# Performance work log

Hardware: AMD Instinct MI355X
Metric: run time of the kernel (lower is better)

The kernel has to match this reference:

```python
import jax, jax.numpy as jnp
import numpy as np

B, N, M, D, NH, HD = 2, 1024, 1024, 1536, 16, 96
RD = HD // 3  # per-axis rotary dim = 32
EPS = 1e-6
SCALE = HD ** -0.5


def _rmsnorm(y, w):
    return y * jax.lax.rsqrt(jnp.mean(y * y, axis=-1, keepdims=True) + EPS) * w


def _rope_tables(T, H, W):
    # inv_freqs identical for t/h/w since all three dims are RD
    inv_f = 1.0 / (10000.0 ** (jnp.arange(0, RD, 2, dtype=jnp.float32)[: RD // 2] / RD))
    gt, gh, gw = jnp.meshgrid(
        jnp.arange(T, dtype=jnp.float32),
        jnp.arange(H, dtype=jnp.float32),
        jnp.arange(W, dtype=jnp.float32),
        indexing='ij')
    ft = gt.reshape(-1, 1) * inv_f[None, :]  # [L, RD//2]
    fh = gh.reshape(-1, 1) * inv_f[None, :]
    fw = gw.reshape(-1, 1) * inv_f[None, :]
    return (jnp.cos(ft), jnp.sin(ft), jnp.cos(fh), jnp.sin(fh), jnp.cos(fw), jnp.sin(fw))


def _apply_rope(xq, cos, sin):
    # xq: [B, L, NH, RD]; cos/sin: [L, RD//2]
    c = jnp.concatenate([cos, cos], axis=-1)[None, :, None, :]
    s = jnp.concatenate([sin, sin], axis=-1)[None, :, None, :]
    x1, x2 = jnp.split(xq, 2, axis=-1)
    rot = jnp.concatenate([-x2, x1], axis=-1)
    return xq * c + rot * s


def setup_inputs() -> dict:
    key = jax.random.key(0)
    ks = jax.random.split(key, 10)
    w = lambda k: jax.random.normal(k, (D, D), dtype=jnp.float32) * 0.02
    return {
        'cond': jax.random.normal(ks[0], (B, N, D), dtype=jnp.float32),
        'x': jax.random.normal(ks[1], (B, M, D), dtype=jnp.float32),
        'cond_q_w': w(ks[2]), 'cond_k_w': w(ks[3]), 'cond_v_w': w(ks[4]),
        'cond_qnorm_w': jnp.ones((D,), jnp.float32),
        'cond_knorm_w': jnp.ones((D,), jnp.float32),
        'cond_proj_w': w(ks[5]),
        'x_q_w': w(ks[6]), 'x_k_w': w(ks[7]), 'x_v_w': w(ks[8]),
        'x_qnorm_w': jnp.ones((D,), jnp.float32),
        'x_knorm_w': jnp.ones((D,), jnp.float32),
        'x_proj_w': w(ks[9]),
        'T': 2, 'H': 32, 'W': 32,
    }


def reference(cond, x, cond_q_w, cond_k_w, cond_v_w, cond_qnorm_w, cond_knorm_w,
              cond_proj_w, x_q_w, x_k_w, x_v_w, x_qnorm_w, x_knorm_w, x_proj_w,
              T, H, W):
    # dual-stream QKV + RMSNorm (qkv_bias=False, eval -> no dropout)
    cq = _rmsnorm(cond @ cond_q_w, cond_qnorm_w).reshape(B, N, NH, HD)
    ck = _rmsnorm(cond @ cond_k_w, cond_knorm_w).reshape(B, N, NH, HD)
    cv = (cond @ cond_v_w).reshape(B, N, NH, HD)
    xq = _rmsnorm(x @ x_q_w, x_qnorm_w).reshape(B, M, NH, HD)
    xk = _rmsnorm(x @ x_k_w, x_knorm_w).reshape(B, M, NH, HD)
    xv = (x @ x_v_w).reshape(B, M, NH, HD)

    q = jnp.concatenate([cq, xq], axis=1)  # [B, N+M, NH, HD]
    k = jnp.concatenate([ck, xk], axis=1)
    v = jnp.concatenate([cv, xv], axis=1)

    # 3D RoPE: split head_dim into t/h/w thirds and rotate each with its own freqs
    cos_t, sin_t, cos_h, sin_h, cos_w, sin_w = _rope_tables(T, H, W)
    qt, qh, qw = jnp.split(q, 3, axis=-1)
    kt, kh, kw = jnp.split(k, 3, axis=-1)
    q = jnp.concatenate([_apply_rope(qt, cos_t, sin_t),
                         _apply_rope(qh, cos_h, sin_h),
                         _apply_rope(qw, cos_w, sin_w)], axis=-1)
    k = jnp.concatenate([_apply_rope(kt, cos_t, sin_t),
                         _apply_rope(kh, cos_h, sin_h),
                         _apply_rope(kw, cos_w, sin_w)], axis=-1)

    # joint non-causal SDPA
    scores = jnp.einsum('blhd,bmhd->bhlm', q, k) * SCALE
    attn = jax.nn.softmax(scores, axis=-1)
    out = jnp.einsum('bhlm,bmhd->blhd', attn, v).reshape(B, N + M, D)

    cond_out = out[:, :N] @ cond_proj_w
    x_out = out[:, N:] @ x_proj_w
    return cond_out, x_out
```

## Files before the change

kernel.cpp:

```cpp
#include <hip/hip_runtime.h>
#include <stdint.h>

#define DEV __device__ __forceinline__

using f32x4  = __attribute__((ext_vector_type(4))) float;
using f32x16 = __attribute__((ext_vector_type(16))) float;
using bf16x8 = __attribute__((ext_vector_type(8))) short;

DEV ushort f2bf(float f){
  uint32_t u = __float_as_uint(f);
  u += 0x7FFFu + ((u >> 16) & 1u);
  return (ushort)(u >> 16);
}
DEV float bf2f(ushort h){ return __uint_as_float(((uint32_t)h) << 16); }

DEV void async16(const void* g, void* l){
  __builtin_amdgcn_global_load_lds(
      (const __attribute__((address_space(1))) void*)g,
      (__attribute__((address_space(3))) void*)l, 16, 0, 0);
}

union FU { uint4 u; bf16x8 v; };
DEV bf16x8 as_bf16x8(uint a, uint b, uint c, uint d){ FU f; f.u = make_uint4(a,b,c,d); return f.v; }

__global__ __launch_bounds__(256) void k_conv_in(const float* __restrict__ src, ushort* __restrict__ dst){
  int i = (blockIdx.x * 256 + threadIdx.x) * 8;
  float4 a = *(const float4*)(src + i);
  float4 b = *(const float4*)(src + i + 4);
  union { ushort s[8]; uint4 q; } o;
  o.s[0]=f2bf(a.x); o.s[1]=f2bf(a.y); o.s[2]=f2bf(a.z); o.s[3]=f2bf(a.w);
  o.s[4]=f2bf(b.x); o.s[5]=f2bf(b.y); o.s[6]=f2bf(b.z); o.s[7]=f2bf(b.w);
  *(uint4*)(dst + i) = o.q;
}

__global__ __launch_bounds__(256) void k_transpose_w(
    const float* w0, const float* w1, const float* w2, const float* w3,
    const float* w4, const float* w5, const float* w6, const float* w7,
    ushort* __restrict__ dst){
  __shared__ float tile[32][33];
  int z = blockIdx.z;
  const float* src = (z==0)?w0:(z==1)?w1:(z==2)?w2:(z==3)?w3:(z==4)?w4:(z==5)?w5:(z==6)?w6:w7;
  int n0 = blockIdx.x * 32;
  int k0 = blockIdx.y * 32;
  int tx = threadIdx.x;
  int ty = threadIdx.y;
  for (int j = 0; j < 4; ++j)
    tile[ty + j*8][tx] = src[(size_t)(k0 + ty + j*8) * 1536 + n0 + tx];
  __syncthreads();
  ushort* d = dst + (size_t)z * 1536 * 1536;
  for (int j = 0; j < 4; ++j){
    int n = n0 + ty + j*8;
    int k = k0 + tx;
    d[(size_t)n * 1536 + k] = f2bf(tile[tx][ty + j*8]);
  }
}

__global__ __launch_bounds__(512, 2) void k_gemm_qkv(const ushort* __restrict__ inb,
                                                     const ushort* __restrict__ Wt,
                                                     ushort* __restrict__ Y){
  __shared__ ushort As[2][16384];
  __shared__ ushort Bs[2][18432];
  int f = blockIdx.x;
  int nid = (f & 7) * 32 + (f >> 3);
  int z = nid >> 7; int r = nid & 127;
  int my = (r >> 2) & 7, nx = (r >> 5) * 4 + (r & 3);
  const ushort* A = inb + (size_t)z * 2048 * 1536 + (size_t)(my * 256) * 1536;
  const ushort* B = Wt  + (size_t)z * 4608 * 1536 + (size_t)(nx * 288) * 1536;
  ushort* Yt = Y + (size_t)z * 2048 * 4608 + (size_t)(my * 256) * 4608 + nx * 288;
  int tid = threadIdx.x;
  int w = tid >> 6, lane = tid & 63;
  int g = lane >> 4, fr = lane & 15;
  int wm = (w >> 1) * 64, wn = (w & 1) * 144;

  f32x4 acc[4][9] = {};

  auto stageA = [&](int b, int kt){
#pragma unroll
    for (int s = 0; s < 4; ++s){
      int c = s * 512 + tid;
      int row = c >> 3, ch = c & 7;
      async16(A + (size_t)row * 1536 + kt + ((ch ^ (row & 7)) * 8), &As[b][(s*512 + w*64) * 8]);
    }
  };
  auto stageB = [&](int b, int kt){
#pragma unroll
    for (int s = 0; s < 4; ++s){
      int c = s * 512 + tid;
      int row = c >> 3, ch = c & 7;
      async16(B + (size_t)row * 1536 + kt + ((ch ^ (row & 7)) * 8), &Bs[b][(s*512 + w*64) * 8]);
    }
    if (tid < 256){
      int c = 2048 + tid;
      int row = c >> 3, ch = c & 7;
      async16(B + (size_t)row * 1536 + kt + ((ch ^ (row & 7)) * 8), &Bs[b][(2048 + w*64) * 8]);
    }
  };

  stageA(0, 0); stageB(0, 0);
  asm volatile("s_waitcnt vmcnt(0)" ::: "memory");
  __builtin_amdgcn_s_barrier();
  asm volatile("" ::: "memory");

  for (int t = 0; t < 24; ++t){
    int cur = t & 1; int kt1 = (t + 1) * 64;
#pragma unroll
    for (int ks = 0; ks < 2; ++ks){
      bf16x8 af[4], bf[9];
#pragma unroll
      for (int j = 0; j < 4; ++j){
        int row = wm + j*16 + fr;
        af[j] = *(const bf16x8*)&As[cur][(row*8 + ((ks*4 + g) ^ (row & 7))) * 8];
      }
#pragma unroll
      for (int ni = 0; ni < 9; ++ni){
        int row = wn + ni*16 + fr;
        bf[ni] = *(const bf16x8*)&Bs[cur][(row*8 + ((ks*4 + g) ^ (row & 7))) * 8];
      }
      if (t < 23){
        if (ks == 0) stageA(cur ^ 1, kt1);
        else stageB(cur ^ 1, kt1);
      }
      asm volatile("" ::: "memory");
      __builtin_amdgcn_s_barrier();
      asm volatile("" ::: "memory");
      __builtin_amdgcn_s_setprio(1);
#pragma unroll
      for (int ni = 0; ni < 9; ++ni){
#pragma unroll
        for (int j = 0; j < 4; ++j)
          acc[j][ni] = __builtin_amdgcn_mfma_f32_16x16x32_bf16(af[j], bf[ni], acc[j][ni], 0, 0, 0);
      }
      __builtin_amdgcn_s_setprio(0);
      if (ks == 1) asm volatile("s_waitcnt vmcnt(0)" ::: "memory");
      asm volatile("" ::: "memory");
      __builtin_amdgcn_s_barrier();
      asm volatile("" ::: "memory");
    }
  }

#pragma unroll
  for (int mi = 0; mi < 4; ++mi)
#pragma unroll
    for (int ni = 0; ni < 9; ++ni)
#pragma unroll
      for (int rr = 0; rr < 4; ++rr)
        Yt[(size_t)(wm + mi*16 + g*4 + rr) * 4608 + wn + ni*16 + fr] = f2bf(acc[mi][ni][rr]);
}

template<bool OUT_BF16>
DEV void gemm_tile(const ushort* __restrict__ A, const ushort* __restrict__ Bt, void* __restrict__ Cp,
                   int K, int lda, int ldb, int ldc, int m0, int n0){
  __shared__ ushort As[8192];
  __shared__ ushort Bs[8192];
  int tid = threadIdx.x;
  int w = tid >> 6, lane = tid & 63;
  int g = lane >> 4, fr = lane & 15;
  int wm = (w >> 1) * 64, wn = (w & 1) * 64;
  f32x4 acc[4][4] = {};
  for (int kt = 0; kt < K; kt += 64){
    __syncthreads();
#pragma unroll
    for (int i = 0; i < 4; ++i){
      int ci = i * 256 + tid;
      int row = ci >> 3, ch = ci & 7;
      int src8 = (ch ^ (row & 7)) * 8;
      async16(A  + (size_t)(m0 + row) * lda + kt + src8, As + (i*256 + w*64) * 8);
      async16(Bt + (size_t)(n0 + row) * ldb + kt + src8, Bs + (i*256 + w*64) * 8);
    }
    __syncthreads();
#pragma unroll
    for (int ks = 0; ks < 2; ++ks){
      bf16x8 af[4], bf[4];
      int cidx = ((ks*4 + g) ^ (fr & 7)) * 8;
#pragma unroll
      for (int mi = 0; mi < 4; ++mi) af[mi] = *(const bf16x8*)(As + (wm + mi*16 + fr) * 64 + cidx);
#pragma unroll
      for (int ni = 0; ni < 4; ++ni) bf[ni] = *(const bf16x8*)(Bs + (wn + ni*16 + fr) * 64 + cidx);
#pragma unroll
      for (int mi = 0; mi < 4; ++mi)
#pragma unroll
        for (int ni = 0; ni < 4; ++ni)
          acc[mi][ni] = __builtin_amdgcn_mfma_f32_16x16x32_bf16(af[mi], bf[ni], acc[mi][ni], 0, 0, 0);
    }
  }
  int cr = (lane >> 4) * 4, cc2 = lane & 15;
#pragma unroll
  for (int mi = 0; mi < 4; ++mi)
#pragma unroll
    for (int ni = 0; ni < 4; ++ni)
#pragma unroll
      for (int r = 0; r < 4; ++r){
        size_t idx = (size_t)(m0 + wm + mi*16 + cr + r) * ldc + (n0 + wn + ni*16 + cc2);
        if (OUT_BF16) ((ushort*)Cp)[idx] = f2bf(acc[mi][ni][r]);
        else          ((float*)Cp)[idx]  = acc[mi][ni][r];
      }
}

__global__ __launch_bounds__(256) void k_gemm_proj(const ushort* __restrict__ AO, const ushort* __restrict__ Wtp,
                                                   float* __restrict__ out){
  int f = blockIdx.x;
  int nid = (f & 7) * 48 + (f >> 3);
  int z = nid / 96; int rr = nid - z * 96;
  int by = rr / 12; int bx = rr - by * 12;
  int s = z >> 1, bb = z & 1;
  gemm_tile<false>(AO + (size_t)(bb*2048 + s*1024) * 1536, Wtp + (size_t)s * 1536 * 1536,
                   (void*)(out + (size_t)(s*2048 + bb*1024) * 1536), 1536, 1536, 1536, 1536,
                   by * 128, bx * 128);
}

__global__ __launch_bounds__(256) void k_norm_rope(
    const ushort* __restrict__ Y,
    const float* __restrict__ qn_c, const float* __restrict__ kn_c,
    const float* __restrict__ qn_x, const float* __restrict__ kn_x,
    ushort* __restrict__ Qb, ushort* __restrict__ Kb, ushort* __restrict__ Vb){
  int r = blockIdx.x;
  int z = blockIdx.y;
  const ushort* y = Y + ((size_t)z * 2048 + r) * 4608;
  const float* qw = z ? qn_x : qn_c;
  const float* kw = z ? kn_x : kn_c;
  int b = r >> 10;
  int l = (z << 10) + (r & 1023);
  int tid = threadIdx.x;
  __shared__ float cs[48], sn[48];
  if (tid < 48){
    int axis = tid >> 4, fj = tid & 15;
    int pos = (axis == 0) ? (l >> 10) : ((axis == 1) ? ((l >> 5) & 31) : (l & 31));
    float inv = __expf(-(float)fj * 0.5756462732485114f);
    float a = (float)pos * inv;
    sn[tid] = sinf(a); cs[tid] = cosf(a);
  }
  float yq1[3], yq2[3], yk1[3], yk2[3];
  float ssq = 0.f, ssk = 0.f;
#pragma unroll
  for (int i = 0; i < 3; ++i){
    int p = tid + i*256;
    int head = p / 48, rem = p % 48;
    int c1 = head*96 + (rem >> 4)*32 + (rem & 15);
    float a1 = bf2f(y[c1]),        a2 = bf2f(y[c1 + 16]);
    float b1 = bf2f(y[1536 + c1]), b2 = bf2f(y[1536 + c1 + 16]);
    yq1[i]=a1; yq2[i]=a2; yk1[i]=b1; yk2[i]=b2;
    ssq += a1*a1 + a2*a2;
    ssk += b1*b1 + b2*b2;
  }
#pragma unroll
  for (int mm = 1; mm < 64; mm <<= 1){
    ssq += __shfl_xor(ssq, mm);
    ssk += __shfl_xor(ssk, mm);
  }
  __shared__ float red[8];
  int w = tid >> 6;
  if ((tid & 63) == 0){ red[w] = ssq; red[4 + w] = ssk; }
  __syncthreads();
  float scq = rsqrtf((red[0]+red[1]+red[2]+red[3]) * (1.f/1536.f) + 1e-6f);
  float sck = rsqrtf((red[4]+red[5]+red[6]+red[7]) * (1.f/1536.f) + 1e-6f);
  float scqS = scq * 0.1020620726159658f;
#pragma unroll
  for (int i = 0; i < 3; ++i){
    int p = tid + i*256;
    int head = p / 48, rem = p % 48;
    int axis = rem >> 4, fj = rem & 15;
    int c1 = head*96 + axis*32 + fj;
    float c = cs[rem], s = sn[rem];
    size_t rowb = ((size_t)(b*16 + head) * 2048 + l) * 96;
    float a1 = yq1[i] * scqS * qw[c1], a2 = yq2[i] * scqS * qw[c1 + 16];
    Qb[rowb + axis*32 + fj]      = f2bf(a1*c - a2*s);
    Qb[rowb + axis*32 + fj + 16] = f2bf(a2*c + a1*s);
    float b1 = yk1[i] * sck * kw[c1], b2 = yk2[i] * sck * kw[c1 + 16];
    int d1 = axis*32 + fj;
    Kb[rowb + d1]      = f2bf(b1*c - b2*s);
    Kb[rowb + d1 + 16] = f2bf(b2*c + b1*s);
  }
#pragma unroll
  for (int i = 0; i < 6; ++i){
    int cidx = tid + i*256;
    int head = cidx / 96, hd = cidx - head*96;
    Vb[((size_t)(b*16 + head) * 2048 + l) * 96 + hd] = y[3072 + cidx];
  }
}

__global__ __launch_bounds__(256) void k_transpose_v(const ushort* __restrict__ V, ushort* __restrict__ Vt){
  __shared__ ushort t[32][33];
  int bh = blockIdx.z;
  const ushort* src = V + (size_t)bh * 2048 * 96;
  ushort* dst = Vt + (size_t)bh * 96 * 2048;
  int c0 = blockIdx.x * 32;
  int r0 = blockIdx.y * 32;
  int tx = threadIdx.x, ty = threadIdx.y;
  for (int j = 0; j < 4; ++j)
    t[ty + j*8][tx] = src[(size_t)(r0 + ty + j*8) * 96 + c0 + tx];
  __syncthreads();
  for (int j = 0; j < 4; ++j){
    int d = c0 + ty + j*8;
    int l = r0 + tx;
    dst[(size_t)d * 2048 + l] = t[tx][ty + j*8];
  }
}

__global__ __launch_bounds__(256, 2) void k_attn(const ushort* __restrict__ Qb, const ushort* __restrict__ Kb,
                                                 const ushort* __restrict__ Vt, ushort* __restrict__ AO){
  __shared__ ushort Ks[64*100];
  __shared__ ushort Vs[96*68];
  int id = blockIdx.x;
  int nid = (id & 7) * 64 + (id >> 3);
  int qt = nid & 15, bh = nid >> 4;
  int b = bh >> 4, head = bh & 15;
  const ushort* Qh = Qb + (size_t)bh * 2048 * 96;
  const ushort* Kh = Kb + (size_t)bh * 2048 * 96;
  const ushort* Vh = Vt + (size_t)bh * 96 * 2048;
  int tid = threadIdx.x;
  int w = tid >> 6, lane = tid & 63;
  int h = lane >> 5, c = lane & 31;
  int q0 = qt * 128 + w * 32;

  bf16x8 qf[6];
#pragma unroll
  for (int kb = 0; kb < 6; ++kb)
    qf[kb] = *(const bf16x8*)(Qh + (size_t)(q0 + c) * 96 + kb*16 + h*8);

  int gko[3], lko[3], gvo[3], lvo[3];
#pragma unroll
  for (int i = 0; i < 3; ++i){
    int fc = i*256 + tid;
    int krow = (fc * 683) >> 13;
    int kc8  = (fc - krow*12) * 8;
    gko[i] = krow*96 + kc8;
    lko[i] = krow*100 + kc8;
    int vrow = fc >> 3;
    int vc8  = (fc & 7) * 8;
    gvo[i] = vrow*2048 + vc8;
    lvo[i] = vrow*68 + (vc8 ^ ((vrow & 7) << 3));
  }
  uint4 kst[3], vst[3];
#pragma unroll
  for (int i = 0; i < 3; ++i){
    kst[i] = *(const uint4*)(Kh + gko[i]);
    vst[i] = *(const uint4*)(Vh + (size_t)gvo[i]);
  }

  f32x16 o[3] = {};
  float dpart = 0.f;

  for (int kt = 0; kt < 32; ++kt){
#pragma unroll
    for (int i = 0; i < 3; ++i){
      *(uint2*)(Ks + lko[i])     = make_uint2(kst[i].x, kst[i].y);
      *(uint2*)(Ks + lko[i] + 4) = make_uint2(kst[i].z, kst[i].w);
      *(uint2*)(Vs + lvo[i])     = make_uint2(vst[i].x, vst[i].y);
      *(uint2*)(Vs + lvo[i] + 4) = make_uint2(vst[i].z, vst[i].w);
    }
    if (kt + 1 < 32){
#pragma unroll
      for (int i = 0; i < 3; ++i){
        kst[i] = *(const uint4*)(Kh + (kt+1)*6144 + gko[i]);
        vst[i] = *(const uint4*)(Vh + (kt+1)*64 + (size_t)gvo[i]);
      }
    }
    asm volatile("s_waitcnt lgkmcnt(0)" ::: "memory");
    __builtin_amdgcn_s_barrier();
    asm volatile("" ::: "memory");

#pragma unroll
    for (int ni = 0; ni < 2; ++ni){
      f32x16 sa = {};
#pragma unroll
      for (int kb = 0; kb < 6; ++kb){
        const ushort* kp = Ks + (ni*32 + c)*100 + kb*16 + h*8;
        uint2 lo = *(const uint2*)kp;
        uint2 hi = *(const uint2*)(kp + 4);
        sa = __builtin_amdgcn_mfma_f32_32x32x16_bf16(as_bf16x8(lo.x, lo.y, hi.x, hi.y), qf[kb], sa, 0, 0, 0);
      }
      float p[16];
#pragma unroll
      for (int e = 0; e < 16; ++e){
        float x = fmaf(sa[e], 1.44269504f, -14.4269504f);
        asm("v_exp_f32 %0, %1" : "=v"(p[e]) : "v"(x));
      }
      dpart += (((p[0]+p[1])+(p[2]+p[3])) + ((p[4]+p[5])+(p[6]+p[7])))
             + (((p[8]+p[9])+(p[10]+p[11])) + ((p[12]+p[13])+(p[14]+p[15])));
      uint u[8];
#pragma unroll
      for (int e = 0; e < 8; ++e)
        asm("v_cvt_pk_bf16_f32 %0, %1, %2" : "=v"(u[e]) : "v"(p[2*e]), "v"(p[2*e+1]));
      asm("v_permlane32_swap_b32 %0, %1" : "+v"(u[0]), "+v"(u[2]));
      asm("v_permlane32_swap_b32 %0, %1" : "+v"(u[1]), "+v"(u[3]));
      asm("v_permlane32_swap_b32 %0, %1" : "+v"(u[4]), "+v"(u[6]));
      asm("v_permlane32_swap_b32 %0, %1" : "+v"(u[5]), "+v"(u[7]));
      bf16x8 pf0 = as_bf16x8(u[0], u[1], u[2], u[3]);
      bf16x8 pf1 = as_bf16x8(u[4], u[5], u[6], u[7]);
#pragma unroll
      for (int dt = 0; dt < 3; ++dt){
#pragma unroll
        for (int ks = 0; ks < 2; ++ks){
          int chunk = 4*ni + 2*ks + h;
          const ushort* vp = Vs + (dt*32 + c)*68 + ((chunk ^ (c & 7)) << 3);
          uint2 lo = *(const uint2*)vp;
          uint2 hi = *(const uint2*)(vp + 4);
          o[dt] = __builtin_amdgcn_mfma_f32_32x32x16_bf16(ks ? pf1 : pf0,
                    as_bf16x8(lo.x, lo.y, hi.x, hi.y), o[dt], 0, 0, 0);
        }
      }
    }
    asm volatile("" ::: "memory");
    __builtin_amdgcn_s_barrier();
    asm volatile("" ::: "memory");
  }

  float dtot = dpart + __shfl_xor(dpart, 32);
#pragma unroll
  for (int r = 0; r < 16; ++r){
    int qloc = (r & 3) + 8*(r >> 2) + 4*h;
    float den = __shfl(dtot, qloc);
    float dinv = __builtin_amdgcn_rcpf(den);
    size_t rowoff = ((size_t)b * 2048 + q0 + qloc) * 1536 + head * 96;
#pragma unroll
    for (int dt = 0; dt < 3; ++dt){
      float val = o[dt][r] * dinv;
      uint pk; asm("v_cvt_pk_bf16_f32 %0, %1, %2" : "=v"(pk) : "v"(val), "v"(val));
      AO[rowoff + dt*32 + c] = (ushort)pk;
    }
  }
}

extern "C" void kernel_launch(void* const* d_in, const int* in_sizes, int n_in,
                              void* d_out, int out_size, void* d_ws, size_t ws_size,
                              hipStream_t stream){
  const float* cond = (const float*)d_in[0];
  const float* x    = (const float*)d_in[1];
  const float* wq_c = (const float*)d_in[2];
  const float* wk_c = (const float*)d_in[3];
  const float* wv_c = (const float*)d_in[4];
  const float* qn_c = (const float*)d_in[5];
  const float* kn_c = (const float*)d_in[6];
  const float* wp_c = (const float*)d_in[7];
  const float* wq_x = (const float*)d_in[8];
  const float* wk_x = (const float*)d_in[9];
  const float* wv_x = (const float*)d_in[10];
  const float* qn_x = (const float*)d_in[11];
  const float* kn_x = (const float*)d_in[12];
  const float* wp_x = (const float*)d_in[13];

  char* ws = (char*)d_ws;
  ushort* inb = (ushort*)(ws);
  ushort* Wt  = (ushort*)(ws + 12582912ll);
  ushort* Y   = (ushort*)(ws + 50331648ll);
  ushort* Vt  = (ushort*)(ws + 50331648ll);
  ushort* Qb  = (ushort*)(ws + 88080384ll);
  ushort* Kb  = (ushort*)(ws + 100663296ll);
  ushort* Vb  = (ushort*)(ws + 113246208ll);
  ushort* AO  = inb;

  k_conv_in<<<1536, 256, 0, stream>>>(cond, inb);
  k_conv_in<<<1536, 256, 0, stream>>>(x, inb + 3145728);
  k_transpose_w<<<dim3(48,48,8), dim3(32,8), 0, stream>>>(wq_c, wk_c, wv_c, wq_x, wk_x, wv_x, wp_c, wp_x, Wt);
  k_gemm_qkv<<<256, 512, 0, stream>>>(inb, Wt, Y);
  k_norm_rope<<<dim3(2048,2), 256, 0, stream>>>(Y, qn_c, kn_c, qn_x, kn_x, Qb, Kb, Vb);
  k_transpose_v<<<dim3(3,64,32), dim3(32,8), 0, stream>>>(Vb, Vt);
  k_attn<<<512, 256, 0, stream>>>(Qb, Kb, Vt, AO);
  k_gemm_proj<<<384, 256, 0, stream>>>(AO, Wt + (size_t)9216*1536, (float*)d_out);
  (void)in_sizes; (void)n_in; (void)out_size; (void)ws_size;
}
```

Baseline: 211.8 us.

## Double-buffer K/V LDS tiles and software-pipeline QK of next tile with PV

The attention kernel now keeps two LDS buffers for K and V, loads global data two tiles ahead, and computes the QK^T scores for tile t+1 while doing the PV MFMAs for tile t. The goal is to overlap the exp/softmax VALU work and LDS waits with MFMA work and hide global load latency. In exchange it doubles LDS use to about 51KB per block and raises register pressure with the extra score accumulators. That may hurt the two-blocks-per-CU occupancy target or cause spills.

```diff
diff --git a/kernel.cpp b/kernel.cpp
--- a/kernel.cpp
+++ b/kernel.cpp
@@ -298,8 +298,8 @@
 
 __global__ __launch_bounds__(256, 2) void k_attn(const ushort* __restrict__ Qb, const ushort* __restrict__ Kb,
                                                  const ushort* __restrict__ Vt, ushort* __restrict__ AO){
-  __shared__ ushort Ks[64*100];
-  __shared__ ushort Vs[96*68];
+  __shared__ ushort Ks[2][6400];
+  __shared__ ushort Vs[2][6528];
   int id = blockIdx.x;
   int nid = (id & 7) * 64 + (id >> 3);
   int qt = nid & 15, bh = nid >> 4;
@@ -331,48 +331,65 @@
     lvo[i] = vrow*68 + (vc8 ^ ((vrow & 7) << 3));
   }
   uint4 kst[3], vst[3];
-#pragma unroll
-  for (int i = 0; i < 3; ++i){
-    kst[i] = *(const uint4*)(Kh + gko[i]);
-    vst[i] = *(const uint4*)(Vh + (size_t)gvo[i]);
-  }
+
+  auto LOADG = [&](int tt){
+#pragma unroll
+    for (int i = 0; i < 3; ++i){
+      kst[i] = *(const uint4*)(Kh + (size_t)tt*6144 + gko[i]);
+      vst[i] = *(const uint4*)(Vh + (size_t)tt*64 + gvo[i]);
+    }
+  };
+  auto WRITE = [&](int buf){
+#pragma unroll
+    for (int i = 0; i < 3; ++i){
+      *(uint2*)(&Ks[buf][lko[i]])     = make_uint2(kst[i].x, kst[i].y);
+      *(uint2*)(&Ks[buf][lko[i] + 4]) = make_uint2(kst[i].z, kst[i].w);
+      *(uint2*)(&Vs[buf][lvo[i]])     = make_uint2(vst[i].x, vst[i].y);
+      *(uint2*)(&Vs[buf][lvo[i] + 4]) = make_uint2(vst[i].z, vst[i].w);
+    }
+  };
+  auto QK = [&](f32x16* sa, int buf){
+#pragma unroll
+    for (int ni = 0; ni < 2; ++ni){
+      f32x16 a = {};
+#pragma unroll
+      for (int kb = 0; kb < 6; ++kb){
+        const ushort* kp = &Ks[buf][(ni*32 + c)*100 + kb*16 + h*8];
+        uint2 lo = *(const uint2*)kp;
+        uint2 hi = *(const uint2*)(kp + 4);
+        a = __builtin_amdgcn_mfma_f32_32x32x16_bf16(as_bf16x8(lo.x, lo.y, hi.x, hi.y), qf[kb], a, 0, 0, 0);
+      }
+      sa[ni] = a;
+    }
+  };
 
   f32x16 o[3] = {};
   float dpart = 0.f;
-
-  for (int kt = 0; kt < 32; ++kt){
-#pragma unroll
-    for (int i = 0; i < 3; ++i){
-      *(uint2*)(Ks + lko[i])     = make_uint2(kst[i].x, kst[i].y);
-      *(uint2*)(Ks + lko[i] + 4) = make_uint2(kst[i].z, kst[i].w);
-      *(uint2*)(Vs + lvo[i])     = make_uint2(vst[i].x, vst[i].y);
-      *(uint2*)(Vs + lvo[i] + 4) = make_uint2(vst[i].z, vst[i].w);
-    }
-    if (kt + 1 < 32){
-#pragma unroll
-      for (int i = 0; i < 3; ++i){
-        kst[i] = *(const uint4*)(Kh + (kt+1)*6144 + gko[i]);
-        vst[i] = *(const uint4*)(Vh + (kt+1)*64 + (size_t)gvo[i]);
-      }
-    }
+  f32x16 sa[2];
+
+  LOADG(0);
+  WRITE(0);
+  LOADG(1);
+  asm volatile("s_waitcnt lgkmcnt(0)" ::: "memory");
+  __builtin_amdgcn_s_barrier();
+  asm volatile("" ::: "memory");
+  QK(sa, 0);
+
+  for (int t = 0; t < 32; ++t){
+    int cur = t & 1, nxt = cur ^ 1;
+    if (t < 31) WRITE(nxt);
+    if (t < 30) LOADG(t + 2);
     asm volatile("s_waitcnt lgkmcnt(0)" ::: "memory");
     __builtin_amdgcn_s_barrier();
     asm volatile("" ::: "memory");
 
+    bf16x8 pf[2][2];
 #pragma unroll
     for (int ni = 0; ni < 2; ++ni){
-      f32x16 sa = {};
-#pragma unroll
-      for (int kb = 0; kb < 6; ++kb){
-        const ushort* kp = Ks + (ni*32 + c)*100 + kb*16 + h*8;
-        uint2 lo = *(const uint2*)kp;
-        uint2 hi = *(const uint2*)(kp + 4);
-        sa = __builtin_amdgcn_mfma_f32_32x32x16_bf16(as_bf16x8(lo.x, lo.y, hi.x, hi.y), qf[kb], sa, 0, 0, 0);
-      }
       float p[16];
 #pragma unroll
       for (int e = 0; e < 16; ++e){
-        float x = fmaf(sa[e], 1.44269504f, -14.4269504f);
+        float x = fmaf(sa[ni][e], 1.44269504f, -14.4269504f);
         asm("v_exp_f32 %0, %1" : "=v"(p[e]) : "v"(x));
       }
       dpart += (((p[0]+p[1])+(p[2]+p[3])) + ((p[4]+p[5])+(p[6]+p[7])))
@@ -385,20 +402,41 @@
       asm("v_permlane32_swap_b32 %0, %1" : "+v"(u[1]), "+v"(u[3]));
       asm("v_permlane32_swap_b32 %0, %1" : "+v"(u[4]), "+v"(u[6]));
       asm("v_permlane32_swap_b32 %0, %1" : "+v"(u[5]), "+v"(u[7]));
-      bf16x8 pf0 = as_bf16x8(u[0], u[1], u[2], u[3]);
-      bf16x8 pf1 = as_bf16x8(u[4], u[5], u[6], u[7]);
-#pragma unroll
-      for (int dt = 0; dt < 3; ++dt){
-#pragma unroll
-        for (int ks = 0; ks < 2; ++ks){
-          int chunk = 4*ni + 2*ks + h;
-          const ushort* vp = Vs + (dt*32 + c)*68 + ((chunk ^ (c & 7)) << 3);
-          uint2 lo = *(const uint2*)vp;
-          uint2 hi = *(const uint2*)(vp + 4);
-          o[dt] = __builtin_amdgcn_mfma_f32_32x32x16_bf16(ks ? pf1 : pf0,
-                    as_bf16x8(lo.x, lo.y, hi.x, hi.y), o[dt], 0, 0, 0);
-        }
-      }
+      pf[ni][0] = as_bf16x8(u[0], u[1], u[2], u[3]);
+      pf[ni][1] = as_bf16x8(u[4], u[5], u[6], u[7]);
+    }
+
+    if (t < 31){
+      f32x16 na[2];
+      QK(na, nxt);
+#pragma unroll
+      for (int dt = 0; dt < 3; ++dt)
+#pragma unroll
+        for (int ni = 0; ni < 2; ++ni)
+#pragma unroll
+          for (int ks = 0; ks < 2; ++ks){
+            int chunk = 4*ni + 2*ks + h;
+            const ushort* vp = &Vs[cur][(dt*32 + c)*68 + ((chunk ^ (c & 7)) << 3)];
+            uint2 lo = *(const uint2*)vp;
+            uint2 hi = *(const uint2*)(vp + 4);
+            o[dt] = __builtin_amdgcn_mfma_f32_32x32x16_bf16(pf[ni][ks],
+                      as_bf16x8(lo.x, lo.y, hi.x, hi.y), o[dt], 0, 0, 0);
+          }
+      sa[0] = na[0]; sa[1] = na[1];
+    } else {
+#pragma unroll
+      for (int dt = 0; dt < 3; ++dt)
+#pragma unroll
+        for (int ni = 0; ni < 2; ++ni)
+#pragma unroll
+          for (int ks = 0; ks < 2; ++ks){
+            int chunk = 4*ni + 2*ks + h;
+            const ushort* vp = &Vs[cur][(dt*32 + c)*68 + ((chunk ^ (c & 7)) << 3)];
+            uint2 lo = *(const uint2*)vp;
+            uint2 hi = *(const uint2*)(vp + 4);
+            o[dt] = __builtin_amdgcn_mfma_f32_32x32x16_bf16(pf[ni][ks],
+                      as_bf16x8(lo.x, lo.y, hi.x, hi.y), o[dt], 0, 0, 0);
+          }
     }
     asm volatile("" ::: "memory");
     __builtin_amdgcn_s_barrier();
```

Measured after the change: 207.6 us. 1.02x faster.
